# Kernel tuning notes

Hardware: AMD Instinct MI355X
Metric: run time of the kernel (lower is better)

The kernel has to match this reference:

```python
import jax, jax.numpy as jnp
import numpy as np

BETA = 0.25
CODEBOOK_SIZE = 4096
DIM = 512


def setup_inputs() -> dict:
    key = jax.random.key(0)
    k1, k2 = jax.random.split(key)
    z_e = jax.random.normal(k1, (16, 1024, 512), dtype=jnp.float32)
    # kaiming_uniform-ish codebook init
    bound = float(np.sqrt(6.0 / ((1.0 + 5.0) * DIM)))
    embed = jax.random.uniform(k2, (CODEBOOK_SIZE, DIM), dtype=jnp.float32,
                               minval=-bound, maxval=bound)
    return {"z_e": z_e, "embed": embed}


def reference(z_e, embed):
    D = embed.shape[1]
    K = embed.shape[0]
    z = z_e.reshape(-1, D)                                   # [N, D]
    N = z.shape[0]
    # squared euclidean distances [N, K]
    distances = (jnp.sum(z * z, axis=1, keepdims=True)
                 - 2.0 * (z @ embed.T)
                 + jnp.sum(embed * embed, axis=1))
    indices = jnp.argmin(distances, axis=1)                  # [N]
    z_q = embed[indices].reshape(z_e.shape)                  # gather == one-hot matmul
    # straight-through estimator
    z_q_st = z_e + jax.lax.stop_gradient(z_q - z_e)
    commitment_loss = jnp.mean((jax.lax.stop_gradient(z_q) - z_e) ** 2)
    vq_loss = BETA * commitment_loss
    # avg_probs = encodings.mean(0) via histogram of indices
    counts = jnp.zeros((K,), dtype=z.dtype).at[indices].add(1.0)
    avg_probs = counts / N
    perplexity = jnp.exp(-jnp.sum(avg_probs * jnp.log(avg_probs + 1e-10)))
    return (z_q_st, indices.reshape(z_e.shape[:-1]), vq_loss, perplexity)
```

## Files before the change

### kernel.cpp

```cpp
#include <hip/hip_runtime.h>
#include <cstdint>
#include <cstddef>

typedef _Float16 f16x8 __attribute__((ext_vector_type(8)));
typedef float f32x4 __attribute__((ext_vector_type(4)));

#define NTOK 16384
#define DIMV 512
#define KCODE 4096

#define IDX_OFF (NTOK * DIMV)
#define LOSSO   (IDX_OFF + NTOK)
#define PERPO   (LOSSO + 1)

static const size_t A2_OFF = 0;
static const size_t B2_OFF = A2_OFF + (size_t)NTOK * DIMV * 2;
static const size_t EN_OFF = B2_OFF + (size_t)KCODE * DIMV * 2;
static const size_t RK_OFF = EN_OFF + (size_t)KCODE * 4;
static const size_t CNT_OFF = RK_OFF + (size_t)NTOK * 32 * 4;
static const size_t RLOSS_OFF = CNT_OFF + (size_t)KCODE * 4;

__device__ __forceinline__ float sqf(float v) {
    float p = v * v;
    asm volatile("" : "+v"(p));
    return p;
}

__device__ __forceinline__ float np_pairwise_sq(const float* xs, int t) {
    float accp = 0.0f;
    if (t < 32) {
        const float* blk = xs + (t >> 3) * 128;
        int j = t & 7;
        float rj = sqf(blk[j]);
#pragma unroll
        for (int tt = 1; tt < 16; ++tt) rj += sqf(blk[tt * 8 + j]);
        accp = rj;
    }
#pragma unroll
    for (int d = 1; d <= 16; d <<= 1) accp += __shfl_xor(accp, d, 64);
    return __shfl(accp, 0, 64);
}

__global__ void prep_k(const float* __restrict__ z, const float* __restrict__ e,
                       _Float16* __restrict__ A2, _Float16* __restrict__ B2,
                       float* __restrict__ C32, unsigned* __restrict__ counts) {
    __shared__ float es[4][512];
    const int b = blockIdx.x;
    if (b < 4096) {
        int t = b * 256 + threadIdx.x;
        int n = t >> 6;
        int dc = (t & 63) << 3;
        const float* zp = z + (size_t)n * DIMV + dc;
        float4 v0 = ((const float4*)zp)[0];
        float4 v1 = ((const float4*)zp)[1];
        float vs[8] = {v0.x, v0.y, v0.z, v0.w, v1.x, v1.y, v1.z, v1.w};
        f16x8 hi;
#pragma unroll
        for (int i = 0; i < 8; ++i) hi[i] = (_Float16)(vs[i] * 256.0f);
        *(f16x8*)(A2 + (size_t)n * DIMV + dc) = hi;
    } else {
        const int wv = threadIdx.x >> 6, t = threadIdx.x & 63;
        const int k = (b - 4096) * 4 + wv;
        const float* ep = e + (size_t)k * DIMV + t * 8;
        float4 v0 = ((const float4*)ep)[0];
        float4 v1 = ((const float4*)ep)[1];
        ((float4*)es[wv])[t * 2] = v0;
        ((float4*)es[wv])[t * 2 + 1] = v1;
        float vs[8] = {v0.x, v0.y, v0.z, v0.w, v1.x, v1.y, v1.z, v1.w};
        f16x8 hi;
#pragma unroll
        for (int i = 0; i < 8; ++i) hi[i] = (_Float16)(vs[i] * 256.0f);
        *(f16x8*)(B2 + (size_t)k * DIMV + t * 8) = hi;
        float c = np_pairwise_sq(es[wv], t);
        if (t == 0) C32[k] = c;
        if (threadIdx.x < 4) counts[(b - 4096) * 4 + threadIdx.x] = 0u;
    }
}

typedef uint32_t __attribute__((address_space(1))) gas_u32;
typedef uint32_t __attribute__((address_space(3))) las_u32;
__device__ __forceinline__ void g2l16(const _Float16* g, _Float16* l) {
    __builtin_amdgcn_global_load_lds((const gas_u32*)(uintptr_t)g,
                                     (las_u32*)(uint32_t)(uintptr_t)l, 16, 0, 0);
}

__device__ __forceinline__ void top2_merge32(unsigned& k1, unsigned& k2,
                                             unsigned o1, unsigned o2) {
    unsigned n1 = k1 < o1 ? k1 : o1;
    unsigned mx = k1 < o1 ? o1 : k1;
    unsigned n2 = k2 < o2 ? k2 : o2;
    k1 = n1;
    k2 = mx < n2 ? mx : n2;
}

#define DPP_TOP2(CTRL)                                                                     \
    {                                                                                      \
        unsigned o1 = (unsigned)__builtin_amdgcn_update_dpp(-1, (int)k1, CTRL, 0xF, 0xF, false); \
        unsigned o2 = (unsigned)__builtin_amdgcn_update_dpp(-1, (int)k2, CTRL, 0xF, 0xF, false); \
        top2_merge32(k1, k2, o1, o2);                                                      \
    }

__global__ __launch_bounds__(512) void gemm_top2_k(
    const _Float16* __restrict__ A2, const _Float16* __restrict__ B2,
    const float* __restrict__ C32, unsigned* __restrict__ rk2) {
    __shared__ _Float16 lA[128 * 64];
    __shared__ _Float16 lB[256 * 64];
    const int nt = blockIdx.x;
    const int mt = blockIdx.y;
    const int tid = threadIdx.x;
    const int w = tid >> 6, l = tid & 63;
    const int wm = w & 1, wn = w >> 1;

    const int srow = l >> 3, schunk = l & 7;
    const int gch = (schunk ^ srow) << 3;
    const _Float16* aG = A2 + (size_t)(mt * 128 + w * 16 + srow) * DIMV + gch;
    const _Float16* bG = B2 + (size_t)(nt * 256 + w * 32 + srow) * DIMV + gch;
    _Float16* aL = &lA[(w * 16) * 64];
    _Float16* bL = &lB[(w * 32) * 64];

    const int lane15 = l & 15, q = l >> 4, sx = l & 7;
    const int aRow = (wm * 64 + lane15) * 64;
    const int bRow = (wn * 64 + lane15) * 64;

    f32x4 acc[4][4] = {};

    for (int kt = 0; kt < 8; ++kt) {
        const _Float16* ag = aG + kt * 64;
        const _Float16* bg = bG + kt * 64;
#pragma unroll
        for (int r = 0; r < 2; ++r) g2l16(ag + (size_t)r * 8 * DIMV, aL + r * 512);
#pragma unroll
        for (int r = 0; r < 4; ++r) g2l16(bg + (size_t)r * 8 * DIMV, bL + r * 512);
        __syncthreads();

#pragma unroll
        for (int kk2 = 0; kk2 < 2; ++kk2) {
            f16x8 af[4], bf[4];
            const int ch = ((kk2 * 4 + q) ^ sx) << 3;
#pragma unroll
            for (int i = 0; i < 4; ++i) {
                af[i] = *(const f16x8*)&lA[aRow + i * 1024 + ch];
                bf[i] = *(const f16x8*)&lB[bRow + i * 1024 + ch];
            }
#pragma unroll
            for (int i = 0; i < 4; ++i)
#pragma unroll
                for (int j = 0; j < 4; ++j)
                    acc[i][j] = __builtin_amdgcn_mfma_f32_16x16x32_f16(af[i], bf[j], acc[i][j], 0, 0, 0);
        }
        __syncthreads();
    }

    unsigned* lk32 = (unsigned*)lA;
    const int colL = wn * 64 + lane15;
    float envals[4];
#pragma unroll
    for (int j = 0; j < 4; ++j) envals[j] = C32[nt * 256 + colL + j * 16] * 65536.0f + 4.0e6f;

#pragma unroll
    for (int i = 0; i < 4; ++i) {
#pragma unroll
        for (int rr = 0; rr < 4; ++rr) {
            unsigned k1 = 0xFFFFFFFFu, k2 = 0xFFFFFFFFu;
#pragma unroll
            for (int j = 0; j < 4; ++j) {
                float dist = envals[j] - 2.0f * acc[i][j][rr];
                unsigned key = (__float_as_uint(dist) & 0xFFFFFF00u) | (unsigned)(colL + j * 16);
                if (key < k1) { k2 = k1; k1 = key; } else if (key < k2) k2 = key;
            }
            DPP_TOP2(0x118)
            DPP_TOP2(0x114)
            DPP_TOP2(0x112)
            DPP_TOP2(0x111)
            if (lane15 == 15) {
                int rl = wm * 64 + i * 16 + q * 4 + rr;
                lk32[rl * 10 + wn * 2]     = k1;
                lk32[rl * 10 + wn * 2 + 1] = k2;
            }
        }
    }
    __syncthreads();
    if (tid < 128) {
        unsigned a1 = lk32[tid * 10], a2 = lk32[tid * 10 + 1];
#pragma unroll
        for (int p = 1; p < 4; ++p)
            top2_merge32(a1, a2, lk32[tid * 10 + p * 2], lk32[tid * 10 + p * 2 + 1]);
        size_t base = (size_t)(mt * 128 + tid) * 32 + nt * 2;
        rk2[base] = a1;
        rk2[base + 1] = a2;
    }
}

__global__ __launch_bounds__(256) void refine_k(
    const unsigned* __restrict__ rk2,
    const float* __restrict__ embed, const float* __restrict__ z,
    const float* __restrict__ C32,
    float* __restrict__ out, unsigned* __restrict__ counts,
    double* __restrict__ rloss) {
    __shared__ float zs[4][512];
    __shared__ float zqs[4][512];
    const int wv = threadIdx.x >> 6, t = threadIdx.x & 63;
    const int r = blockIdx.x * 4 + wv;
    const float4* zp = (const float4*)(z + (size_t)r * DIMV);
    float4 za = zp[t * 2], zb = zp[t * 2 + 1];
    ((float4*)zs[wv])[t * 2] = za;
    ((float4*)zs[wv])[t * 2 + 1] = zb;
    __syncthreads();

    float A32 = np_pairwise_sq(zs[wv], t);

    unsigned long long key = ~0ull;
    if (t < 32) {
        unsigned kraw = rk2[(size_t)r * 32 + t];
        unsigned col = (unsigned)(t >> 1) * 256u + (kraw & 255u);
        key = ((unsigned long long)(kraw & 0xFFFFFF00u) << 32) | col;
    }

    const int g = t >> 4, j = t & 15;
    unsigned mycand = 0;
#pragma unroll
    for (int c = 0; c < 4; ++c) {
        unsigned long long m = key;
#pragma unroll
        for (int d = 1; d < 64; d <<= 1) {
            unsigned long long o = __shfl_xor(m, d, 64);
            m = o < m ? o : m;
        }
        if (c == g) mycand = (unsigned)(m & 0xFFFFFFFFull);
        if (key == m) key = ~0ull;
    }

    const float4* ep = (const float4*)(embed + (size_t)mycand * DIMV);
    float4 ev[8];
    double s = 0.0;
#pragma unroll
    for (int it = 0; it < 8; ++it) {
        float4 e4 = ep[j + it * 16];
        ev[it] = e4;
        float4 z4 = ((const float4*)zs[wv])[j + it * 16];
        s += (double)z4.x * e4.x + (double)z4.y * e4.y +
             (double)z4.z * e4.z + (double)z4.w * e4.w;
    }
#pragma unroll
    for (int d = 1; d < 16; d <<= 1) s += __shfl_xor(s, d, 64);

    float Bf = (float)s;
    float d32 = (A32 - 2.0f * Bf) + C32[mycand];
    unsigned u = __float_as_uint(d32);
    u = (u & 0x80000000u) ? ~u : (u | 0x80000000u);
    unsigned long long dk = ((unsigned long long)u << 32) | mycand;
#pragma unroll
    for (int d = 16; d < 64; d <<= 1) {
        unsigned long long o = __shfl_xor(dk, d, 64);
        dk = o < dk ? o : dk;
    }
    const unsigned ibest = (unsigned)(dk & 0xFFFFFFFFull);

    if (mycand == ibest) {
#pragma unroll
        for (int it = 0; it < 8; ++it) ((float4*)zqs[wv])[j + it * 16] = ev[it];
    }
    __syncthreads();

    float4 wa = ((const float4*)zqs[wv])[t * 2];
    float4 wb = ((const float4*)zqs[wv])[t * 2 + 1];
    float4* op = (float4*)(out + (size_t)r * DIMV);
    op[t * 2] = wa;
    op[t * 2 + 1] = wb;
    double dx0 = (double)za.x - wa.x, dx1 = (double)za.y - wa.y;
    double dx2 = (double)za.z - wa.z, dx3 = (double)za.w - wa.w;
    double dx4 = (double)zb.x - wb.x, dx5 = (double)zb.y - wb.y;
    double dx6 = (double)zb.z - wb.z, dx7 = (double)zb.w - wb.w;
    double ls = dx0 * dx0 + dx1 * dx1 + dx2 * dx2 + dx3 * dx3 +
                dx4 * dx4 + dx5 * dx5 + dx6 * dx6 + dx7 * dx7;
#pragma unroll
    for (int d = 1; d < 64; d <<= 1) ls += __shfl_xor(ls, d, 64);
    if (t == 0) {
        out[IDX_OFF + r] = (float)ibest;
        rloss[r] = ls;
        atomicAdd(&counts[ibest], 1u);
    }
}

__global__ __launch_bounds__(1024) void scalars_k(
    const unsigned* __restrict__ counts,
    const double* __restrict__ rloss, float* __restrict__ out) {
    int t = threadIdx.x;
    double ls = 0.0;
    for (int i = t; i < NTOK; i += 1024) ls += rloss[i];
#pragma unroll
    for (int d = 1; d < 64; d <<= 1) ls += __shfl_xor(ls, d, 64);
    float s = 0.0f;
    for (int i = t; i < KCODE; i += 1024) {
        float p = (float)counts[i] * (1.0f / (float)NTOK);
        s += p * logf(p + 1e-10f);
    }
#pragma unroll
    for (int d = 1; d < 64; d <<= 1) s += __shfl_xor(s, d, 64);
    __shared__ float red[16];
    __shared__ double redd[16];
    if ((t & 63) == 0) { red[t >> 6] = s; redd[t >> 6] = ls; }
    __syncthreads();
    if (t == 0) {
        float stot = 0.0f;
        double ltot = 0.0;
#pragma unroll
        for (int i = 0; i < 16; ++i) { stot += red[i]; ltot += redd[i]; }
        out[PERPO] = expf(-stot);
        out[LOSSO] = 0.25f * (float)(ltot * (1.0 / (double)(NTOK * DIMV)));
    }
}

extern "C" void kernel_launch(void* const* d_in, const int* in_sizes, int n_in,
                              void* d_out, int out_size, void* d_ws, size_t ws_size,
                              hipStream_t stream) {
    const float* z     = (const float*)d_in[0];
    const float* embed = (const float*)d_in[1];
    float* out = (float*)d_out;
    char* ws = (char*)d_ws;

    _Float16* A2 = (_Float16*)(ws + A2_OFF);
    _Float16* B2 = (_Float16*)(ws + B2_OFF);
    float* C32 = (float*)(ws + EN_OFF);
    unsigned* rk2 = (unsigned*)(ws + RK_OFF);
    unsigned* counts = (unsigned*)(ws + CNT_OFF);
    double* rloss = (double*)(ws + RLOSS_OFF);

    prep_k<<<5120, 256, 0, stream>>>(z, embed, A2, B2, C32, counts);
    gemm_top2_k<<<dim3(16, 128), 512, 0, stream>>>(A2, B2, C32, rk2);
    refine_k<<<NTOK / 4, 256, 0, stream>>>(rk2, embed, z, C32, out, counts, rloss);
    scalars_k<<<1, 1024, 0, stream>>>(counts, rloss, out);
}
```

Measured before the change: 209.2 us.

## Double-buffer LDS and enlarge GEMM tile to 256x256 with phased prefetch

```diff
diff --git a/kernel.cpp b/kernel.cpp
--- a/kernel.cpp
+++ b/kernel.cpp
@@ -100,71 +100,93 @@
         top2_merge32(k1, k2, o1, o2);                                                      \
     }
 
-__global__ __launch_bounds__(512) void gemm_top2_k(
+#define PHASE(MH, KS, LOADB, STAGE_CALL)                                           \
+    {                                                                              \
+        f16x8 af[4];                                                               \
+        _Pragma("unroll") for (int i = 0; i < 4; ++i)                              \
+            af[i] = *(const f16x8*)&L[bb + (KS)*8192 + aOff + ((MH)*4 + i) * 512]; \
+        if (LOADB) {                                                               \
+            _Pragma("unroll") for (int j = 0; j < 4; ++j)                          \
+                bf[j] = *(const f16x8*)&L[bb + (KS)*8192 + bOff + j * 512];        \
+        }                                                                          \
+        STAGE_CALL;                                                                \
+        __builtin_amdgcn_s_setprio(1);                                             \
+        _Pragma("unroll") for (int i = 0; i < 4; ++i)                              \
+            _Pragma("unroll") for (int j = 0; j < 4; ++j)                          \
+                acc[(MH)*4 + i][j] = __builtin_amdgcn_mfma_f32_16x16x32_f16(       \
+                    af[i], bf[j], acc[(MH)*4 + i][j], 0, 0, 0);                    \
+        __builtin_amdgcn_s_setprio(0);                                             \
+    }
+
+__global__ __launch_bounds__(512, 2) void gemm_top2_k(
     const _Float16* __restrict__ A2, const _Float16* __restrict__ B2,
     const float* __restrict__ C32, unsigned* __restrict__ rk2) {
-    __shared__ _Float16 lA[128 * 64];
-    __shared__ _Float16 lB[256 * 64];
+    __shared__ __align__(16) _Float16 L[65536];
+
     const int nt = blockIdx.x;
     const int mt = blockIdx.y;
     const int tid = threadIdx.x;
     const int w = tid >> 6, l = tid & 63;
-    const int wm = w & 1, wn = w >> 1;
-
-    const int srow = l >> 3, schunk = l & 7;
-    const int gch = (schunk ^ srow) << 3;
-    const _Float16* aG = A2 + (size_t)(mt * 128 + w * 16 + srow) * DIMV + gch;
-    const _Float16* bG = B2 + (size_t)(nt * 256 + w * 32 + srow) * DIMV + gch;
-    _Float16* aL = &lA[(w * 16) * 64];
-    _Float16* bL = &lB[(w * 32) * 64];
-
-    const int lane15 = l & 15, q = l >> 4, sx = l & 7;
-    const int aRow = (wm * 64 + lane15) * 64;
-    const int bRow = (wn * 64 + lane15) * 64;
-
-    f32x4 acc[4][4] = {};
-
-    for (int kt = 0; kt < 8; ++kt) {
-        const _Float16* ag = aG + kt * 64;
-        const _Float16* bg = bG + kt * 64;
-#pragma unroll
-        for (int r = 0; r < 2; ++r) g2l16(ag + (size_t)r * 8 * DIMV, aL + r * 512);
-#pragma unroll
-        for (int r = 0; r < 4; ++r) g2l16(bg + (size_t)r * 8 * DIMV, bL + r * 512);
-        __syncthreads();
-
-#pragma unroll
-        for (int kk2 = 0; kk2 < 2; ++kk2) {
-            f16x8 af[4], bf[4];
-            const int ch = ((kk2 * 4 + q) ^ sx) << 3;
-#pragma unroll
-            for (int i = 0; i < 4; ++i) {
-                af[i] = *(const f16x8*)&lA[aRow + i * 1024 + ch];
-                bf[i] = *(const f16x8*)&lB[bRow + i * 1024 + ch];
-            }
-#pragma unroll
-            for (int i = 0; i < 4; ++i)
-#pragma unroll
-                for (int j = 0; j < 4; ++j)
-                    acc[i][j] = __builtin_amdgcn_mfma_f32_16x16x32_f16(af[i], bf[j], acc[i][j], 0, 0, 0);
-        }
-        __syncthreads();
-    }
-
-    unsigned* lk32 = (unsigned*)lA;
+    const int wm = w >> 2, wn = w & 3;
+    const int lane15 = l & 15, q = l >> 4;
+
+    const int lo = l >> 2;
+    const int cswz = (l & 3) ^ ((l >> 3) & 3);
+    const _Float16* aSrc0 = A2 + (size_t)(mt * 256 + w * 16 + lo) * DIMV + cswz * 8;
+    const _Float16* aSrc1 = A2 + (size_t)(mt * 256 + 128 + w * 16 + lo) * DIMV + cswz * 8;
+    const _Float16* bSrc0 = B2 + (size_t)(nt * 256 + w * 16 + lo) * DIMV + cswz * 8;
+    const _Float16* bSrc1 = B2 + (size_t)(nt * 256 + 128 + w * 16 + lo) * DIMV + cswz * 8;
+
+    auto stageA = [&](int nb_, int kh, int kt) {
+        g2l16(aSrc0 + kt * 64 + kh * 32, &L[nb_ + kh * 8192 + w * 512]);
+        g2l16(aSrc1 + kt * 64 + kh * 32, &L[nb_ + kh * 8192 + 4096 + w * 512]);
+    };
+    auto stageB = [&](int nb_, int kh, int kt) {
+        g2l16(bSrc0 + kt * 64 + kh * 32, &L[nb_ + 16384 + kh * 8192 + w * 512]);
+        g2l16(bSrc1 + kt * 64 + kh * 32, &L[nb_ + 16384 + kh * 8192 + 4096 + w * 512]);
+    };
+
+    const int slot8 = (q ^ ((lane15 >> 1) & 3)) * 8;
+    const int aOff = (wm * 128 + lane15) * 32 + slot8;
+    const int bOff = 16384 + (wn * 64 + lane15) * 32 + slot8;
+
+    f32x4 acc[8][4] = {};
+    f16x8 bf[4];
+
+    stageA(0, 0, 0); stageB(0, 0, 0); stageA(0, 1, 0); stageB(0, 1, 0);
+
+    for (int t = 0; t < 8; ++t) {
+        const int bb = (t & 1) << 15;
+        const int nb = ((t + 1) & 1) << 15;
+        const bool pf = t < 7;
+        asm volatile("s_waitcnt vmcnt(4)" ::: "memory");
+        __builtin_amdgcn_s_barrier();
+        PHASE(0, 0, true, if (pf) stageA(nb, 0, t + 1))
+        __builtin_amdgcn_s_barrier();
+        PHASE(1, 0, false, if (pf) stageB(nb, 0, t + 1))
+        if (pf) { asm volatile("s_waitcnt vmcnt(4)" ::: "memory"); }
+        else    { asm volatile("s_waitcnt vmcnt(0)" ::: "memory"); }
+        __builtin_amdgcn_s_barrier();
+        PHASE(0, 1, true, if (pf) stageA(nb, 1, t + 1))
+        __builtin_amdgcn_s_barrier();
+        PHASE(1, 1, false, if (pf) stageB(nb, 1, t + 1))
+    }
+    __builtin_amdgcn_s_barrier();
+
+    unsigned* lk32 = (unsigned*)L;
     const int colL = wn * 64 + lane15;
     float envals[4];
 #pragma unroll
     for (int j = 0; j < 4; ++j) envals[j] = C32[nt * 256 + colL + j * 16] * 65536.0f + 4.0e6f;
 
 #pragma unroll
-    for (int i = 0; i < 4; ++i) {
+    for (int mf = 0; mf < 8; ++mf) {
 #pragma unroll
         for (int rr = 0; rr < 4; ++rr) {
             unsigned k1 = 0xFFFFFFFFu, k2 = 0xFFFFFFFFu;
 #pragma unroll
             for (int j = 0; j < 4; ++j) {
-                float dist = envals[j] - 2.0f * acc[i][j][rr];
+                float dist = envals[j] - 2.0f * acc[mf][j][rr];
                 unsigned key = (__float_as_uint(dist) & 0xFFFFFF00u) | (unsigned)(colL + j * 16);
                 if (key < k1) { k2 = k1; k1 = key; } else if (key < k2) k2 = key;
             }
@@ -173,19 +195,19 @@
             DPP_TOP2(0x112)
             DPP_TOP2(0x111)
             if (lane15 == 15) {
-                int rl = wm * 64 + i * 16 + q * 4 + rr;
+                int rl = wm * 128 + mf * 16 + q * 4 + rr;
                 lk32[rl * 10 + wn * 2]     = k1;
                 lk32[rl * 10 + wn * 2 + 1] = k2;
             }
         }
     }
     __syncthreads();
-    if (tid < 128) {
+    if (tid < 256) {
         unsigned a1 = lk32[tid * 10], a2 = lk32[tid * 10 + 1];
 #pragma unroll
         for (int p = 1; p < 4; ++p)
             top2_merge32(a1, a2, lk32[tid * 10 + p * 2], lk32[tid * 10 + p * 2 + 1]);
-        size_t base = (size_t)(mt * 128 + tid) * 32 + nt * 2;
+        size_t base = (size_t)(mt * 256 + tid) * 32 + nt * 2;
         rk2[base] = a1;
         rk2[base + 1] = a2;
     }
@@ -327,7 +349,7 @@
     double* rloss = (double*)(ws + RLOSS_OFF);
 
     prep_k<<<5120, 256, 0, stream>>>(z, embed, A2, B2, C32, counts);
-    gemm_top2_k<<<dim3(16, 128), 512, 0, stream>>>(A2, B2, C32, rk2);
+    gemm_top2_k<<<dim3(16, 64), 512, 0, stream>>>(A2, B2, C32, rk2);
     refine_k<<<NTOK / 4, 256, 0, stream>>>(rk2, embed, z, C32, out, counts, rloss);
     scalars_k<<<1, 1024, 0, stream>>>(counts, rloss, out);
 }
```

Result: no change. 213.1 us (+1.9%).
